# Kernel tuning notes

Measured on AMD Instinct MI355X. Metric: run time of the kernel, lower is better.

## Reference

```python
import jax, jax.numpy as jnp
import numpy as np
from jax import lax

BITS = 8
STRIDE = 1
PADDING = 1
SCALE = 2.0 ** (BITS - 1)  # fixed-point scale 2^(bits-1)


def setup_inputs() -> dict:
    key = jax.random.key(0)
    k1, k2, k3 = jax.random.split(key, 3)
    x = jax.random.normal(k1, (32, 128, 56, 56), dtype=jnp.float32)
    W = jax.random.normal(k2, (256, 128, 3, 3), dtype=jnp.float32)
    b = jax.random.normal(k3, (256,), dtype=jnp.float32)
    return {"x": x, "W": W, "b": b}


def reference(x, W, b):
    # to_fix_point: round(v * 2^(bits-1)); torch keeps long ints, but all
    # arithmetic in forward promotes back to float, so float round is exact here.
    w_q = jnp.round(W * SCALE)
    b_q = jnp.round(b * SCALE)
    # calConv: out[i,j] = sum(patch * w_q) / 2^(bits-1) + b_q
    # (square 3x3 kernel makes the original's transposed patch indexing a standard conv)
    out = lax.conv_general_dilated(
        x, w_q,
        window_strides=(STRIDE, STRIDE),
        padding=[(PADDING, PADDING), (PADDING, PADDING)],
        dimension_numbers=("NCHW", "OIHW", "NCHW"),
    )
    return out / SCALE + b_q[None, :, None, None]
```

## Files before the change

### kernel.cpp

```cpp
#include <hip/hip_runtime.h>

typedef _Float16 half8 __attribute__((ext_vector_type(8)));
typedef float floatx4 __attribute__((ext_vector_type(4)));

#define IMG   3136
#define PIMG  3364
#define XP_ELEMS (32 * 58 * 58 * 128)
#define WQ_ELEMS (9 * 256 * 128)

__global__ __launch_bounds__(256) void pad_x_kernel(const float* __restrict__ x,
                                                    _Float16* __restrict__ xp) {
    const int hh = blockIdx.x;
    const int n  = blockIdx.y;
    const int t  = threadIdx.x;
    _Float16* rowbase = xp + ((long)(n * 58 + hh) * 58) * 128;

    if (hh == 0 || hh == 57) {
        #pragma unroll
        for (int i = 0; i < 4; ++i) {
            int idx = i * 256 + t;
            if (idx < 928) *(half8*)(rowbase + idx * 8) = (half8)(_Float16)0.0f;
        }
        return;
    }

    __shared__ _Float16 tile[128 * 57];
    const int h = hh - 1;

    #pragma unroll
    for (int p = 0; p < 7; ++p) {
        int idx = p * 256 + t;
        int c   = idx / 14;
        int w4  = (idx % 14) * 4;
        const float4 v = *(const float4*)(x + ((long)(n * 128 + c) * 56 + h) * 56 + w4);
        _Float16* d = tile + c * 57 + w4;
        d[0] = (_Float16)v.x; d[1] = (_Float16)v.y;
        d[2] = (_Float16)v.z; d[3] = (_Float16)v.w;
    }
    __syncthreads();

    #pragma unroll
    for (int p = 0; p < 4; ++p) {
        int idx = p * 256 + t;
        if (idx < 896) {
            int ww = idx >> 4;
            int c0 = (idx & 15) * 8;
            half8 v;
            #pragma unroll
            for (int j = 0; j < 8; ++j) v[j] = tile[(c0 + j) * 57 + ww];
            *(half8*)(rowbase + (ww + 1) * 128 + c0) = v;
        }
    }
    if (t < 32) {
        int ww = (t >> 4) ? 57 : 0;
        int c0 = (t & 15) * 8;
        *(half8*)(rowbase + ww * 128 + c0) = (half8)(_Float16)0.0f;
    }
}

__global__ void quant_w_kernel(const float* __restrict__ W, _Float16* __restrict__ wq) {
    int t = blockIdx.x * 256 + threadIdx.x;
    int c  = t & 127;
    int k  = (t >> 7) & 255;
    int rs = t >> 15;
    wq[t] = (_Float16)rintf(W[(k * 128 + c) * 9 + rs] * 128.0f);
}

__global__ __launch_bounds__(256) void conv_mfma_kernel(
    const _Float16* __restrict__ xp, const _Float16* __restrict__ wq,
    const float* __restrict__ b, float* __restrict__ out)
{
    __shared__ __align__(16) _Float16 smem[8192];
    _Float16* As = smem;
    _Float16* Bs = smem + 4096;

    const int tid = threadIdx.x;
    const int l   = tid & 63;
    const int wv  = tid >> 6;
    const int wm  = wv & 1;
    const int wn  = wv >> 1;
    const int bx  = blockIdx.x;
    const int by  = blockIdx.y;

    const int lrow = l >> 2;
    const int lcol = (((l & 3) ^ ((l >> 3) & 3))) * 8;

    const int kf0   = by * 128 + wv * 16 + lrow;
    const int aoff0 = kf0 * 128 + lcol;
    const int aoff1 = aoff0 + 64 * 128;

    const int pix0 = bx * 128 + wv * 16 + lrow;
    const int pix1 = pix0 + 64;
    const int n0 = pix0 / IMG, hw0 = pix0 % IMG;
    const int n1 = pix1 / IMG, hw1 = pix1 % IMG;
    const int pb0 = (n0 * PIMG + (hw0 / 56) * 58 + (hw0 % 56)) * 128 + lcol;
    const int pb1 = (n1 * PIMG + (hw1 / 56) * 58 + (hw1 % 56)) * 128 + lcol;

    _Float16* AsW = As + wv * 512;
    _Float16* BsW = Bs + wv * 512;

    floatx4 acc[4][4] = {};

    for (int rs = 0; rs < 9; ++rs) {
        const _Float16* wg = wq + rs * (256 * 128);
        const _Float16* xg = xp + ((rs / 3) * 58 + (rs % 3)) * 128;
        #pragma unroll 1
        for (int cc = 0; cc < 4; ++cc) {
            const int co = cc * 32;
            __builtin_amdgcn_global_load_lds((__attribute__((address_space(1))) void*)(wg + aoff0 + co),
                                             (__attribute__((address_space(3))) void*)(AsW), 16, 0, 0);
            __builtin_amdgcn_global_load_lds((__attribute__((address_space(1))) void*)(wg + aoff1 + co),
                                             (__attribute__((address_space(3))) void*)(AsW + 2048), 16, 0, 0);
            __builtin_amdgcn_global_load_lds((__attribute__((address_space(1))) void*)(xg + pb0 + co),
                                             (__attribute__((address_space(3))) void*)(BsW), 16, 0, 0);
            __builtin_amdgcn_global_load_lds((__attribute__((address_space(1))) void*)(xg + pb1 + co),
                                             (__attribute__((address_space(3))) void*)(BsW + 2048), 16, 0, 0);
            __syncthreads();

            half8 af[4], bf[4];
            const int ar = wm * 64 + (l & 15);
            const int br = wn * 64 + (l & 15);
            const int kq = (((l >> 4) ^ ((l >> 1) & 3))) * 8;
            #pragma unroll
            for (int mi = 0; mi < 4; ++mi)
                af[mi] = *(const half8*)(As + (ar + mi * 16) * 32 + kq);
            #pragma unroll
            for (int ni = 0; ni < 4; ++ni)
                bf[ni] = *(const half8*)(Bs + (br + ni * 16) * 32 + kq);
            #pragma unroll
            for (int mi = 0; mi < 4; ++mi)
                #pragma unroll
                for (int ni = 0; ni < 4; ++ni)
                    acc[mi][ni] = __builtin_amdgcn_mfma_f32_16x16x32_f16(af[mi], bf[ni], acc[mi][ni], 0, 0, 0);
            __syncthreads();
        }
    }

    #pragma unroll
    for (int mi = 0; mi < 4; ++mi) {
        const int kb = by * 128 + wm * 64 + mi * 16 + (l >> 4) * 4;
        #pragma unroll
        for (int rg = 0; rg < 4; ++rg) {
            const int k = kb + rg;
            const float bq = rintf(b[k] * 128.0f);
            #pragma unroll
            for (int ni = 0; ni < 4; ++ni) {
                const int pix = bx * 128 + wn * 64 + ni * 16 + (l & 15);
                const int n  = pix / IMG;
                const int pr = pix - n * IMG;
                out[((long)n * 256 + k) * IMG + pr] = acc[mi][ni][rg] * (1.0f / 128.0f) + bq;
            }
        }
    }
}

__global__ void conv_fallback_kernel(const float* __restrict__ x, const float* __restrict__ W,
                                     const float* __restrict__ b, float* __restrict__ out)
{
    __shared__ float wsm[1152];
    const int k = blockIdx.y;
    for (int i = threadIdx.x; i < 1152; i += 256)
        wsm[i] = rintf(W[k * 1152 + i] * 128.0f);
    __syncthreads();
    const int pix = blockIdx.x * 256 + threadIdx.x;
    const int n = pix / IMG, hw = pix % IMG;
    const int h = hw / 56, w = hw % 56;
    float acc = 0.0f;
    for (int c = 0; c < 128; ++c) {
        const float* xr = x + ((n * 128 + c) * 56) * 56;
        const float* wr = wsm + c * 9;
        #pragma unroll
        for (int r = 0; r < 3; ++r) {
            const int hh = h + r - 1;
            if ((unsigned)hh >= 56u) continue;
            #pragma unroll
            for (int s = 0; s < 3; ++s) {
                const int ww = w + s - 1;
                if ((unsigned)ww >= 56u) continue;
                acc += xr[hh * 56 + ww] * wr[r * 3 + s];
            }
        }
    }
    out[((long)n * 256 + k) * IMG + hw] = acc * (1.0f / 128.0f) + rintf(b[k] * 128.0f);
}

extern "C" void kernel_launch(void* const* d_in, const int* in_sizes, int n_in,
                              void* d_out, int out_size, void* d_ws, size_t ws_size,
                              hipStream_t stream) {
    const float* x = (const float*)d_in[0];
    const float* W = (const float*)d_in[1];
    const float* b = (const float*)d_in[2];
    float* out = (float*)d_out;

    const size_t need = (size_t)XP_ELEMS * 2 + (size_t)WQ_ELEMS * 2;
    if (ws_size >= need) {
        _Float16* xp = (_Float16*)d_ws;
        _Float16* wq = xp + XP_ELEMS;
        pad_x_kernel<<<dim3(58, 32), 256, 0, stream>>>(x, xp);
        quant_w_kernel<<<WQ_ELEMS / 256, 256, 0, stream>>>(W, wq);
        conv_mfma_kernel<<<dim3(784, 2), 256, 0, stream>>>(xp, wq, b, out);
    } else {
        conv_fallback_kernel<<<dim3(392, 256), 256, 0, stream>>>(x, W, b, out);
    }
}
```

Before: 225.7 us.

## Double-buffer LDS tiles to overlap global loads with MFMA compute

Doubles the shared-memory buffer and restructures the 9x4 reduction loop into a flat 36-step software pipeline. The next stage's global-to-LDS loads are issued before computing the current stage, using a partial vmcnt wait plus raw barriers. This aims to hide global load latency behind MFMA work. The cost is twice the LDS per block, which may reduce occupancy, and it relies on hand-written waitcnt and barrier ordering for correctness.

```diff
diff --git a/kernel.cpp b/kernel.cpp
--- a/kernel.cpp
+++ b/kernel.cpp
@@ -7,6 +7,9 @@
 #define PIMG  3364
 #define XP_ELEMS (32 * 58 * 58 * 128)
 #define WQ_ELEMS (9 * 256 * 128)
+
+#define AS1 __attribute__((address_space(1)))
+#define AS3 __attribute__((address_space(3)))
 
 __global__ __launch_bounds__(256) void pad_x_kernel(const float* __restrict__ x,
                                                     _Float16* __restrict__ xp) {
@@ -70,9 +73,7 @@
     const _Float16* __restrict__ xp, const _Float16* __restrict__ wq,
     const float* __restrict__ b, float* __restrict__ out)
 {
-    __shared__ __align__(16) _Float16 smem[8192];
-    _Float16* As = smem;
-    _Float16* Bs = smem + 4096;
+    __shared__ __align__(16) _Float16 smem[16384];
 
     const int tid = threadIdx.x;
     const int l   = tid & 63;
@@ -83,10 +84,9 @@
     const int by  = blockIdx.y;
 
     const int lrow = l >> 2;
-    const int lcol = (((l & 3) ^ ((l >> 3) & 3))) * 8;
-
-    const int kf0   = by * 128 + wv * 16 + lrow;
-    const int aoff0 = kf0 * 128 + lcol;
+    const int lcol = ((l & 3) ^ ((l >> 3) & 3)) * 8;
+
+    const int aoff0 = (by * 128 + wv * 16 + lrow) * 128 + lcol;
     const int aoff1 = aoff0 + 64 * 128;
 
     const int pix0 = bx * 128 + wv * 16 + lrow;
@@ -96,45 +96,59 @@
     const int pb0 = (n0 * PIMG + (hw0 / 56) * 58 + (hw0 % 56)) * 128 + lcol;
     const int pb1 = (n1 * PIMG + (hw1 / 56) * 58 + (hw1 % 56)) * 128 + lcol;
 
-    _Float16* AsW = As + wv * 512;
-    _Float16* BsW = Bs + wv * 512;
+    const int stageoff = wv * 512;
 
     floatx4 acc[4][4] = {};
 
-    for (int rs = 0; rs < 9; ++rs) {
+    auto issue = [&](int t, int pbuf) {
+        const int rs = t >> 2;
+        const int cc = t & 3;
+        const int r  = (rs * 11) >> 5;
+        const int s2 = rs - r * 3;
         const _Float16* wg = wq + rs * (256 * 128);
-        const _Float16* xg = xp + ((rs / 3) * 58 + (rs % 3)) * 128;
-        #pragma unroll 1
-        for (int cc = 0; cc < 4; ++cc) {
-            const int co = cc * 32;
-            __builtin_amdgcn_global_load_lds((__attribute__((address_space(1))) void*)(wg + aoff0 + co),
-                                             (__attribute__((address_space(3))) void*)(AsW), 16, 0, 0);
-            __builtin_amdgcn_global_load_lds((__attribute__((address_space(1))) void*)(wg + aoff1 + co),
-                                             (__attribute__((address_space(3))) void*)(AsW + 2048), 16, 0, 0);
-            __builtin_amdgcn_global_load_lds((__attribute__((address_space(1))) void*)(xg + pb0 + co),
-                                             (__attribute__((address_space(3))) void*)(BsW), 16, 0, 0);
-            __builtin_amdgcn_global_load_lds((__attribute__((address_space(1))) void*)(xg + pb1 + co),
-                                             (__attribute__((address_space(3))) void*)(BsW + 2048), 16, 0, 0);
-            __syncthreads();
-
-            half8 af[4], bf[4];
-            const int ar = wm * 64 + (l & 15);
-            const int br = wn * 64 + (l & 15);
-            const int kq = (((l >> 4) ^ ((l >> 1) & 3))) * 8;
-            #pragma unroll
-            for (int mi = 0; mi < 4; ++mi)
-                af[mi] = *(const half8*)(As + (ar + mi * 16) * 32 + kq);
+        const _Float16* xg = xp + (r * 58 + s2) * 128;
+        const int co = cc * 32;
+        _Float16* A = smem + pbuf * 8192 + stageoff;
+        _Float16* B = smem + pbuf * 8192 + 4096 + stageoff;
+        __builtin_amdgcn_global_load_lds((AS1 void*)(wg + aoff0 + co), (AS3 void*)A,          16, 0, 0);
+        __builtin_amdgcn_global_load_lds((AS1 void*)(wg + aoff1 + co), (AS3 void*)(A + 2048), 16, 0, 0);
+        __builtin_amdgcn_global_load_lds((AS1 void*)(xg + pb0  + co), (AS3 void*)B,          16, 0, 0);
+        __builtin_amdgcn_global_load_lds((AS1 void*)(xg + pb1  + co), (AS3 void*)(B + 2048), 16, 0, 0);
+    };
+
+    const int ar = wm * 64 + (l & 15);
+    const int br = wn * 64 + (l & 15);
+    const int kq = ((l >> 4) ^ ((l >> 1) & 3)) * 8;
+
+    auto compute = [&](int pbuf) {
+        const _Float16* As = smem + pbuf * 8192;
+        const _Float16* Bs = As + 4096;
+        half8 af[4], bf[4];
+        #pragma unroll
+        for (int mi = 0; mi < 4; ++mi)
+            af[mi] = *(const half8*)(As + (ar + mi * 16) * 32 + kq);
+        #pragma unroll
+        for (int ni = 0; ni < 4; ++ni)
+            bf[ni] = *(const half8*)(Bs + (br + ni * 16) * 32 + kq);
+        #pragma unroll
+        for (int mi = 0; mi < 4; ++mi)
             #pragma unroll
             for (int ni = 0; ni < 4; ++ni)
-                bf[ni] = *(const half8*)(Bs + (br + ni * 16) * 32 + kq);
-            #pragma unroll
-            for (int mi = 0; mi < 4; ++mi)
-                #pragma unroll
-                for (int ni = 0; ni < 4; ++ni)
-                    acc[mi][ni] = __builtin_amdgcn_mfma_f32_16x16x32_f16(af[mi], bf[ni], acc[mi][ni], 0, 0, 0);
-            __syncthreads();
-        }
-    }
+                acc[mi][ni] = __builtin_amdgcn_mfma_f32_16x16x32_f16(af[mi], bf[ni], acc[mi][ni], 0, 0, 0);
+    };
+
+    issue(0, 0);
+    #pragma unroll 2
+    for (int s = 0; s < 35; ++s) {
+        issue(s + 1, (s + 1) & 1);
+        asm volatile("s_waitcnt vmcnt(4)" ::: "memory");
+        asm volatile("s_barrier" ::: "memory");
+        compute(s & 1);
+        asm volatile("s_barrier" ::: "memory");
+    }
+    asm volatile("s_waitcnt vmcnt(0)" ::: "memory");
+    asm volatile("s_barrier" ::: "memory");
+    compute(1);
 
     #pragma unroll
     for (int mi = 0; mi < 4; ++mi) {
```

After: 212.9 us. -5.7%, faster.
